# Performance work log

Hardware: AMD Instinct MI355X
Metric: run time of the kernel (lower is better)

## Reference

```python
import jax, jax.numpy as jnp
import numpy as np

EMB_DIM, TREE_DIM, OUT_DIM, VOCAB = 256, 256, 3, 10000
T, B, LEVELS = 255, 128, 8  # complete binary tree of depth 8, 128 trees per input


def _build_forest():
    # node j = T-1-heap(j): root (heap 0) is the LAST node so stack_last_h picks the root.
    heap = np.arange(T)
    depth = np.floor(np.log2(heap + 1)).astype(np.int64)  # 0..7
    node_order = np.empty(T, dtype=np.int64)
    node_order[T - 1 - heap] = (LEVELS - 1) - depth       # leaves=0, root=7
    internal = np.arange((T - 1) // 2)                     # heaps with two children
    parent = np.repeat(T - 1 - internal, 2)
    child = np.stack([T - 1 - (2 * internal + 1), T - 1 - (2 * internal + 2)], 1).reshape(-1)
    edges = np.stack([parent, child], axis=1)              # (254, 2)
    edge_order = node_order[parent]
    offs = (np.arange(B) * T)[:, None, None]
    adj = (edges[None] + offs).reshape(-1, 2)              # (B*254, 2)
    return np.tile(node_order, B), adj, np.tile(edge_order, B)


def setup_inputs() -> dict:
    key = jax.random.key(0)
    ks = jax.random.split(key, 16)
    no, adj, eo = _build_forest()
    D = TREE_DIM
    s_e = 1.0 / np.sqrt(EMB_DIM)
    s_t = 1.0 / np.sqrt(D)
    return {
        'feat_cube': jax.random.randint(ks[0], (B * T,), 0, VOCAB),
        'feat_a': jax.random.randint(ks[1], (B * T,), 0, VOCAB),
        'feat_b': jax.random.randint(ks[2], (B * T,), 0, VOCAB),
        'node_order': jnp.asarray(no),
        'adjacency_list': jnp.asarray(adj),
        'edge_order': jnp.asarray(eo),
        'num_levels': LEVELS,
        'num_trees': B,
        'emb': jax.random.normal(ks[3], (VOCAB, EMB_DIM), jnp.float32),
        'W_iou': jax.random.normal(ks[4], (3 * D, EMB_DIM), jnp.float32) * s_e,
        'b_iou': jnp.zeros((3 * D,), jnp.float32),
        'U_iou': jax.random.normal(ks[5], (3 * D, D), jnp.float32) * s_t,
        'W_f': jax.random.normal(ks[6], (D, EMB_DIM), jnp.float32) * s_e,
        'b_f': jnp.zeros((D,), jnp.float32),
        'U_f': jax.random.normal(ks[7], (D, D), jnp.float32) * s_t,
        'fc1_w': jax.random.normal(ks[8], (D // 2, D), jnp.float32) * s_t,
        'fc1_b': jnp.zeros((D // 2,), jnp.float32),
        'fc2_w': jax.random.normal(ks[9], (OUT_DIM, D // 2), jnp.float32) * (1.0 / np.sqrt(D // 2)),
        'fc2_b': jnp.zeros((OUT_DIM,), jnp.float32),
    }


def _tree_lstm(x, node_order, parents, children, edge_order, W_iou, b_iou, U_iou, W_f, b_f, U_f, num_levels):
    # Child-sum TreeLSTM, evaluated level by level (leaves first). Dense masked
    # formulation: per level we update only nodes with node_order==lvl; edge
    # contributions are masked before segment_sum (same math as the torch loop).
    N = x.shape[0]
    D = U_f.shape[0]
    x_iou = x @ W_iou.T + b_iou            # (N, 3D), precomputed once
    x_f = x @ W_f.T + b_f                  # (N, D)
    h = jnp.zeros((N, D), x.dtype)
    c = jnp.zeros((N, D), x.dtype)
    for lvl in range(num_levels):
        emask = (edge_order == lvl)[:, None].astype(x.dtype)
        ch = h[children]                   # (E, D) gather of child hidden
        cc = c[children]
        f = jax.nn.sigmoid(x_f[parents] + ch @ U_f.T)
        h_sum = jax.ops.segment_sum(ch * emask, parents, num_segments=N)
        c_sum = jax.ops.segment_sum(f * cc * emask, parents, num_segments=N)
        i, o, u = jnp.split(x_iou + h_sum @ U_iou.T, 3, axis=1)
        c_new = jax.nn.sigmoid(i) * jnp.tanh(u) + c_sum
        h_new = jax.nn.sigmoid(o) * jnp.tanh(c_new)
        nmask = (node_order == lvl)[:, None]
        h = jnp.where(nmask, h_new, h)
        c = jnp.where(nmask, c_new, c)
    return h, c


def reference(feat_cube, feat_a, feat_b, node_order, adjacency_list, edge_order,
              num_levels, num_trees, emb, W_iou, b_iou, U_iou, W_f, b_f, U_f,
              fc1_w, fc1_b, fc2_w, fc2_b):
    parents = adjacency_list[:, 0]
    children = adjacency_list[:, 1]

    def run_tree(feat):
        h, _ = _tree_lstm(emb[feat], node_order, parents, children, edge_order,
                          W_iou, b_iou, U_iou, W_f, b_f, U_f, num_levels)
        # stack_last_h: last node of each tree (= root with our labeling)
        return h.reshape(num_trees, -1, h.shape[-1])[:, -1, :]

    h_c = run_tree(feat_cube)
    h_a = run_tree(feat_a)
    h_b = run_tree(feat_b)
    # h_c (1,D) @ (h_a (D,1) @ h_b (1,D)) == (h_c . h_a) * h_b, fused einsum
    h = jnp.einsum('bi,bi,bj->bj', h_c, h_a, h_b)
    hid = jax.nn.relu(h @ fc1_w.T + fc1_b)
    logits = jax.nn.relu(hid @ fc2_w.T + fc2_b)
    return logits  # (num_trees, out_dim)
```

## Files before the change

### kernel.cpp

```cpp
#include <hip/hip_runtime.h>
#include <hip/hip_bf16.h>

typedef __hip_bfloat16 bf16;
typedef unsigned short u16;
typedef __attribute__((ext_vector_type(8))) short s8;
typedef __attribute__((ext_vector_type(4))) float f4;

#define NRUNS 3
#define NTREE 128
#define TT    255
#define DD    256
#define VPAD  10016
#define PAD   258
#define OPAD  264
#define FPAD  264

__device__ __forceinline__ float bits2f(u16 b){ union{unsigned u; float f;} x; x.u = ((unsigned)b)<<16; return x.f; }
__device__ __forceinline__ u16   f2bits(float f){ bf16 h = __float2bfloat16(f); return *(u16*)&h; }
__device__ __forceinline__ float sigm(float x){ return 1.f/(1.f+__expf(-x)); }
__device__ __forceinline__ float tanh_(float x){ return 1.f - 2.f/(__expf(2.f*x)+1.f); }

__global__ void k_detect(const u16* __restrict__ raw, int* __restrict__ flag){
    int t = threadIdx.x;
    int hit = 0;
    if (t < 128){
        u16 w = raw[2*t];
        int e = (w >> 7) & 0xFF;
        hit = (e >= 100 && e <= 141) ? 1 : 0;
    }
    __shared__ int cnt;
    if (t == 0) cnt = 0;
    __syncthreads();
    atomicAdd(&cnt, hit);
    __syncthreads();
    if (t == 0) flag[0] = (cnt >= 64) ? 1 : 0;
}

__device__ __forceinline__ u16 cvt1b(const void* p, int i, int isb){
    return isb ? ((const u16*)p)[i] : f2bits(((const float*)p)[i]);
}
__device__ __forceinline__ float cvt1f(const void* p, int i, int isb){
    return isb ? bits2f(((const u16*)p)[i]) : ((const float*)p)[i];
}

#define L_EMB  (10000*256)
#define L_EMBP (VPAD*256)
#define L_WIOU (768*256)
#define L_UIOU (768*256)
#define L_WF   (256*256)
#define L_UF   (256*256)
#define L_ALL  (L_EMBP + L_WIOU + L_UIOU + L_WF + L_UF)
__global__ void k_cvtb(const void* __restrict__ s0, const void* __restrict__ s1,
                       const void* __restrict__ s2, const void* __restrict__ s3,
                       const void* __restrict__ s4,
                       u16* __restrict__ d0, u16* __restrict__ d1, u16* __restrict__ d2,
                       u16* __restrict__ d3, u16* __restrict__ d4,
                       const int* __restrict__ flag){
    int isb = flag[0];
    for (int i = blockIdx.x*blockDim.x + threadIdx.x; i < L_ALL; i += gridDim.x*blockDim.x){
        int j = i;
        if (j < L_EMBP){ d0[j] = (j < L_EMB) ? cvt1b(s0, j, isb) : (u16)0; continue; } j -= L_EMBP;
        if (j < L_WIOU){ d1[j] = cvt1b(s1, j, isb); continue; } j -= L_WIOU;
        if (j < L_UIOU){ d2[j] = cvt1b(s2, j, isb); continue; } j -= L_UIOU;
        if (j < L_WF){ d3[j] = cvt1b(s3, j, isb); continue; } j -= L_WF;
        d4[j] = cvt1b(s4, j, isb);
    }
}

#define S_BIOU 768
#define S_BF   256
#define S_F1W  (128*256)
#define S_F1B  128
#define S_F2W  (3*128)
#define S_F2B  3
#define S_ALL  (S_BIOU+S_BF+S_F1W+S_F1B+S_F2W+S_F2B)
__global__ void k_small(const void* __restrict__ s0, const void* __restrict__ s1,
                        const void* __restrict__ s2, const void* __restrict__ s3,
                        const void* __restrict__ s4, const void* __restrict__ s5,
                        float* __restrict__ d0, float* __restrict__ d1, float* __restrict__ d2,
                        float* __restrict__ d3, float* __restrict__ d4, float* __restrict__ d5,
                        const int* __restrict__ flag){
    int isb = flag[0];
    for (int i = blockIdx.x*blockDim.x + threadIdx.x; i < S_ALL; i += gridDim.x*blockDim.x){
        int j = i;
        if (j < S_BIOU){ d0[j] = cvt1f(s0, j, isb); continue; } j -= S_BIOU;
        if (j < S_BF){ d1[j] = cvt1f(s1, j, isb); continue; } j -= S_BF;
        if (j < S_F1W){ d2[j] = cvt1f(s2, j, isb); continue; } j -= S_F1W;
        if (j < S_F1B){ d3[j] = cvt1f(s3, j, isb); continue; } j -= S_F1B;
        if (j < S_F2W){ d4[j] = cvt1f(s4, j, isb); continue; } j -= S_F2W;
        d5[j] = cvt1f(s5, j, isb);
    }
}

__device__ __forceinline__ s8 ldB16(const u16* p){
    union { uint4 q; s8 v; } u;
    u.q = *(const uint4*)p;
    return u.v;
}
__device__ __forceinline__ s8 ldsA(const u16* p){
    union { unsigned w[4]; s8 v; } u;
    u.w[0] = *(const unsigned*)(p);
    u.w[1] = *(const unsigned*)(p+2);
    u.w[2] = *(const unsigned*)(p+4);
    u.w[3] = *(const unsigned*)(p+6);
    return u.v;
}
#define MFMA(acc,a,b) acc = __builtin_amdgcn_mfma_f32_16x16x32_bf16(a, b, acc, 0, 0, 0)

__global__ __launch_bounds__(512, 4)
void k_vocab2(const u16* __restrict__ embb,
              const u16* __restrict__ Wiou, const u16* __restrict__ Wfm,
              const u16* __restrict__ Ufm,  const float* __restrict__ biou_f,
              u16* __restrict__ E4, u16* __restrict__ E_f,
              u16* __restrict__ H0, u16* __restrict__ C0, u16* __restrict__ HU0)
{
    __shared__ u16 hs[32*PAD];
    const int t = threadIdx.x, w = t>>6, lane = t&63, ln = lane&15, q = lane>>4;
    const int r0 = blockIdx.x*32, d0 = w*32;

    const u16* Bp[8];
    #pragma unroll
    for (int g = 0; g < 4; g++)
      #pragma unroll
      for (int nc = 0; nc < 2; nc++){
        int nn = d0 + nc*16 + ln;
        Bp[g*2+nc] = (g < 3) ? (Wiou + (size_t)(g*256+nn)*DD) : (Wfm + (size_t)nn*DD);
      }
    const u16* a0p = embb + (size_t)(r0+ln)*DD;
    const u16* a1p = embb + (size_t)(r0+16+ln)*DD;
    f4 acc[8][2];
    #pragma unroll
    for (int nt = 0; nt < 8; nt++){ acc[nt][0] = (f4){0,0,0,0}; acc[nt][1] = (f4){0,0,0,0}; }
    #pragma unroll 2
    for (int ks = 0; ks < 8; ks++){
        int ko = ks*32 + q*8;
        s8 a0 = ldB16(a0p + ko);
        s8 a1 = ldB16(a1p + ko);
        #pragma unroll
        for (int nt = 0; nt < 8; nt++){
            s8 bb = ldB16(Bp[nt] + ko);
            MFMA(acc[nt][0], a0, bb);
            MFMA(acc[nt][1], a1, bb);
        }
    }
    #pragma unroll
    for (int nc = 0; nc < 2; nc++){
        int d = d0 + nc*16 + ln;
        float bi = biou_f[d], bo = biou_f[256+d], bu = biou_f[512+d];
        #pragma unroll
        for (int ms = 0; ms < 2; ms++)
          #pragma unroll
          for (int r = 0; r < 4; r++){
            int vrow = r0 + ms*16 + q*4 + r;
            float ei = acc[0*2+nc][ms][r];
            float eo = acc[1*2+nc][ms][r];
            float eu = acc[2*2+nc][ms][r];
            float ef = acc[3*2+nc][ms][r];
            union { u16 a[4]; uint2 q2; } pk;
            pk.a[0] = f2bits(ei);
            pk.a[1] = f2bits(eo);
            pk.a[2] = f2bits(eu);
            pk.a[3] = f2bits(ef);
            *(uint2*)(E4 + ((size_t)vrow*DD + d)*4) = pk.q2;
            E_f[(size_t)vrow*DD + d] = f2bits(ef);
            float cc = sigm(ei + bi)*tanh_(eu + bu);
            float hh = sigm(eo + bo)*tanh_(cc);
            C0[(size_t)vrow*DD + d] = f2bits(cc);
            H0[(size_t)vrow*DD + d] = f2bits(hh);
            hs[(ms*16 + q*4 + r)*PAD + d] = f2bits(hh);
        }
    }
    __syncthreads();

    f4 hacc[2][2];
    #pragma unroll
    for (int nt = 0; nt < 2; nt++){ hacc[nt][0] = (f4){0,0,0,0}; hacc[nt][1] = (f4){0,0,0,0}; }
    const u16* Bf0 = Ufm + (size_t)(d0 + ln)*DD;
    const u16* Bf1 = Ufm + (size_t)(d0 + 16 + ln)*DD;
    #pragma unroll 2
    for (int ks = 0; ks < 8; ks++){
        int ko = ks*32 + q*8;
        s8 a0 = ldsA(&hs[ln*PAD + ko]);
        s8 a1 = ldsA(&hs[(16+ln)*PAD + ko]);
        s8 b0 = ldB16(Bf0 + ko);
        s8 b1 = ldB16(Bf1 + ko);
        MFMA(hacc[0][0], a0, b0); MFMA(hacc[0][1], a1, b0);
        MFMA(hacc[1][0], a0, b1); MFMA(hacc[1][1], a1, b1);
    }
    #pragma unroll
    for (int nc = 0; nc < 2; nc++){
        int d = d0 + nc*16 + ln;
        #pragma unroll
        for (int ms = 0; ms < 2; ms++)
          #pragma unroll
          for (int r = 0; r < 4; r++){
            int vrow = r0 + ms*16 + q*4 + r;
            HU0[(size_t)vrow*DD + d] = f2bits(hacc[nc][ms][r]);
        }
    }
}

__global__ __launch_bounds__(512, 4)
void k_edge0(const int* __restrict__ f0, const int* __restrict__ f1, const int* __restrict__ f2,
             const u16* __restrict__ E_f, const u16* __restrict__ H0,
             const u16* __restrict__ C0,  const u16* __restrict__ HU0,
             const float* __restrict__ bf_f,
             u16* __restrict__ hsum_out, u16* __restrict__ fcsum_out)
{
    int gid = blockIdx.x*512 + threadIdx.x;
    int row = gid >> 5, ch = gid & 31, d = ch*8;
    int run = row >> 13, rem = row & 8191, b = rem >> 6, jj = rem & 63;
    const int* fp = (run==0) ? f0 : ((run==1) ? f1 : f2);
    int fo = fp[b*TT + 128 + jj];
    int v1 = fp[b*TT + 2*jj];
    int v2 = fp[b*TT + 2*jj + 1];
    s8 ef  = ldB16(E_f + (size_t)fo*DD + d);
    s8 hu1 = ldB16(HU0 + (size_t)v1*DD + d);
    s8 hu2 = ldB16(HU0 + (size_t)v2*DD + d);
    s8 c1  = ldB16(C0  + (size_t)v1*DD + d);
    s8 c2  = ldB16(C0  + (size_t)v2*DD + d);
    s8 h1  = ldB16(H0  + (size_t)v1*DD + d);
    s8 h2  = ldB16(H0  + (size_t)v2*DD + d);
    union { u16 a[8]; uint4 q4; } uh, uf;
    #pragma unroll
    for (int j = 0; j < 8; j++){
        float e  = bits2f((u16)ef[j]) + bf_f[d+j];
        float fa = sigm(e + bits2f((u16)hu1[j]));
        float fb = sigm(e + bits2f((u16)hu2[j]));
        float fc = fa*bits2f((u16)c1[j]) + fb*bits2f((u16)c2[j]);
        float hsv = bits2f((u16)h1[j]) + bits2f((u16)h2[j]);
        uf.a[j] = f2bits(fc);
        uh.a[j] = f2bits(hsv);
    }
    *(uint4*)(hsum_out  + (size_t)row*DD + d) = uh.q4;
    *(uint4*)(fcsum_out + (size_t)row*DD + d) = uf.q4;
}

__global__ __launch_bounds__(512, 4)
void k_lvl(int lvl, int cLog,
           const int* __restrict__ f0, const int* __restrict__ f1, const int* __restrict__ f2,
           const u16* __restrict__ E4, const u16* __restrict__ E_f,
           const u16* __restrict__ Uiou, const u16* __restrict__ Ufm,
           const float* __restrict__ biou_f, const float* __restrict__ bf_f,
           const u16* __restrict__ hsum_in, const u16* __restrict__ fcsum_in,
           u16* __restrict__ hsum_out, u16* __restrict__ fcsum_out,
           u16* __restrict__ hroot)
{
    __shared__ u16 hs[32*PAD];
    __shared__ u16 hso[16*OPAD];
    __shared__ u16 fco[16*OPAD];
    __shared__ int sfr[32];
    const int t = threadIdx.x, w = t>>6, lane = t&63, ln = lane&15, q = lane>>4;
    const int cnt = 1 << cLog, S = 256 - 2*cnt;
    const int r0 = blockIdx.x*32, d0 = w*32;
    const bool haveP = (lvl < 7);

    if (t < 32){
        int rho = r0 + t;
        int run = rho >> (7+cLog);
        int rem = rho & ((1<<(7+cLog)) - 1);
        int b = rem >> cLog, jj = rem & (cnt-1);
        const int* fp = (run==0) ? f0 : ((run==1) ? f1 : f2);
        sfr[t] = fp[b*TT + S + jj];
    }

    int featp[2][2];
    if (haveP){
        #pragma unroll
        for (int ms = 0; ms < 2; ms++)
          #pragma unroll
          for (int rr = 0; rr < 2; rr++){
            int rho = r0 + ms*16 + q*4 + rr*2;
            int run = rho >> (7+cLog);
            int rem = rho & ((1<<(7+cLog)) - 1);
            int b = rem >> cLog, jj = rem & (cnt-1);
            const int* fp = (run==0) ? f0 : ((run==1) ? f1 : f2);
            featp[ms][rr] = fp[b*TT + (256-cnt) + (jj>>1)];
          }
    }
    __syncthreads();

    f4 acc[6][2];
    #pragma unroll
    for (int nt = 0; nt < 6; nt++){ acc[nt][0] = (f4){0,0,0,0}; acc[nt][1] = (f4){0,0,0,0}; }
    {
        const u16* a0p = hsum_in + (size_t)(r0+ln)*DD;
        const u16* a1p = hsum_in + (size_t)(r0+16+ln)*DD;
        const u16* Bp[6];
        #pragma unroll
        for (int nt = 0; nt < 6; nt++){
            int n = (nt>>1)*256 + d0 + (nt&1)*16 + ln;
            Bp[nt] = Uiou + (size_t)n*DD;
        }
        #pragma unroll 2
        for (int ks = 0; ks < 8; ks++){
            int ko = ks*32 + q*8;
            s8 a0 = ldB16(a0p + ko);
            s8 a1 = ldB16(a1p + ko);
            #pragma unroll
            for (int nt = 0; nt < 6; nt++){
                s8 bb = ldB16(Bp[nt] + ko);
                MFMA(acc[nt][0], a0, bb);
                MFMA(acc[nt][1], a1, bb);
            }
        }
    }

    float cv[2][2][4];
    #pragma unroll
    for (int nc = 0; nc < 2; nc++){
        int d = d0 + nc*16 + ln;
        float bi = biou_f[d], bo = biou_f[256+d], bu = biou_f[512+d];
        #pragma unroll
        for (int ms = 0; ms < 2; ms++){
            float hv[4];
            #pragma unroll
            for (int r = 0; r < 4; r++){
                int m   = ms*16 + q*4 + r;
                int rho = r0 + m;
                union { uint2 q2; u16 a[4]; } ev;
                ev.q2 = *(const uint2*)(E4 + ((size_t)sfr[m]*DD + d)*4);
                float iv = acc[0+nc][ms][r] + bits2f(ev.a[0]) + bi;
                float ov = acc[2+nc][ms][r] + bits2f(ev.a[1]) + bo;
                float uv = acc[4+nc][ms][r] + bits2f(ev.a[2]) + bu;
                float cs = bits2f(fcsum_in[(size_t)rho*DD + d]);
                float c = sigm(iv)*tanh_(uv) + cs;
                float h = sigm(ov)*tanh_(c);
                cv[nc][ms][r] = c;
                hv[r] = h;
                if (haveP) hs[m*PAD + d] = f2bits(h);
                else       hroot[(size_t)rho*DD + d] = f2bits(h);
            }
            if (haveP){
                int lr = ms*8 + q*2;
                hso[lr*OPAD + d]     = f2bits(hv[0] + hv[1]);
                hso[(lr+1)*OPAD + d] = f2bits(hv[2] + hv[3]);
            }
        }
    }

    if (haveP){
        __syncthreads();
        f4 hacc[2][2];
        #pragma unroll
        for (int nt = 0; nt < 2; nt++){ hacc[nt][0] = (f4){0,0,0,0}; hacc[nt][1] = (f4){0,0,0,0}; }
        const u16* Bf0 = Ufm + (size_t)(d0 + ln)*DD;
        const u16* Bf1 = Ufm + (size_t)(d0 + 16 + ln)*DD;
        #pragma unroll 2
        for (int ks = 0; ks < 8; ks++){
            int ko = ks*32 + q*8;
            s8 a0 = ldsA(&hs[ln*PAD + ko]);
            s8 a1 = ldsA(&hs[(16+ln)*PAD + ko]);
            s8 b0 = ldB16(Bf0 + ko);
            s8 b1 = ldB16(Bf1 + ko);
            MFMA(hacc[0][0], a0, b0); MFMA(hacc[0][1], a1, b0);
            MFMA(hacc[1][0], a0, b1); MFMA(hacc[1][1], a1, b1);
        }
        #pragma unroll
        for (int nc = 0; nc < 2; nc++){
            int d = d0 + nc*16 + ln;
            float bfv = bf_f[d];
            #pragma unroll
            for (int ms = 0; ms < 2; ms++){
                float fs0, fs1;
                #pragma unroll
                for (int r = 0; r < 4; r++){
                    float ef = bits2f(E_f[(size_t)featp[ms][r>>1]*DD + d]);
                    float fc = sigm(ef + bfv + hacc[nc][ms][r]) * cv[nc][ms][r];
                    if (r == 0) fs0 = fc;
                    else if (r == 1) fs0 += fc;
                    else if (r == 2) fs1 = fc;
                    else fs1 += fc;
                }
                int lr = ms*8 + q*2;
                fco[lr*OPAD + d]     = f2bits(fs0);
                fco[(lr+1)*OPAD + d] = f2bits(fs1);
            }
        }

        __syncthreads();
        {
            int row = t >> 5, c = (t & 31) * 8;
            int prow = (r0 >> 1) + row;
            uint4 vh = *(const uint4*)&hso[row*OPAD + c];
            uint4 vf = *(const uint4*)&fco[row*OPAD + c];
            *(uint4*)(hsum_out  + (size_t)prow*DD + c) = vh;
            *(uint4*)(fcsum_out + (size_t)prow*DD + c) = vf;
        }
    }
}

__global__ __launch_bounds__(1024, 4)
void k_tail(const int* __restrict__ f0, const int* __restrict__ f1, const int* __restrict__ f2,
            const u16* __restrict__ E4, const u16* __restrict__ E_f,
            const u16* __restrict__ Uiou, const u16* __restrict__ Ufm,
            const float* __restrict__ biou_f, const float* __restrict__ bf_f,
            const u16* __restrict__ hsum_in, const u16* __restrict__ fcsum_in,
            u16* __restrict__ hroot)
{
    __shared__ u16 hs[32*PAD];
    __shared__ u16 hsP[2][32*PAD];
    __shared__ u16 fcP[2][32*FPAD];
    __shared__ int sf[64];
    const int t = threadIdx.x, w = t>>6, lane = t&63, ln = lane&15, q = lane>>4;
    const int d0 = w*16;
    const int d  = d0 + ln;
    const int r0 = blockIdx.x*32;
    const int run = (blockIdx.x*4) >> 7;
    const int* __restrict__ fp = (run==0) ? f0 : ((run==1) ? f1 : f2);

    if (t < 64){
        int ti = t >> 4, idx = t & 15;
        int b = (blockIdx.x*4 + ti) & 127;
        sf[t] = (idx < 15) ? fp[b*TT + 240 + idx] : 0;
    }
    __syncthreads();

    const u16* Bp[3];
    #pragma unroll
    for (int g = 0; g < 3; g++)
        Bp[g] = Uiou + (size_t)(g*256 + d0 + ln)*DD;
    const u16* Bf0 = Ufm + (size_t)(d0 + ln)*DD;

    const float bi = biou_f[d], bo = biou_f[256+d], bu = biou_f[512+d];
    const float bfv = bf_f[d];

    for (int l = 4; l <= 7; l++){
        const int nl = 128 >> l;
        const int nrows = 4*nl;
        const int sh = 7 - l;
        const int inb = (l-1) & 1, outb = l & 1;
        const bool haveP = (l < 7);

        f4 acc[3][2];
        #pragma unroll
        for (int nt = 0; nt < 3; nt++){ acc[nt][0] = (f4){0,0,0,0}; acc[nt][1] = (f4){0,0,0,0}; }
        if (l == 4){
            const u16* a0p = hsum_in + (size_t)(r0+ln)*DD;
            const u16* a1p = hsum_in + (size_t)(r0+16+ln)*DD;
            #pragma unroll 2
            for (int ks = 0; ks < 8; ks++){
                int ko = ks*32 + q*8;
                s8 a0 = ldB16(a0p + ko);
                s8 a1 = ldB16(a1p + ko);
                #pragma unroll
                for (int nt = 0; nt < 3; nt++){
                    s8 bb = ldB16(Bp[nt] + ko);
                    MFMA(acc[nt][0], a0, bb);
                    MFMA(acc[nt][1], a1, bb);
                }
            }
        } else {
            const u16* a0l = &hsP[inb][ln*PAD];
            const u16* a1l = &hsP[inb][(16+ln)*PAD];
            #pragma unroll 2
            for (int ks = 0; ks < 8; ks++){
                int ko = ks*32 + q*8;
                s8 a0 = ldsA(a0l + ko);
                s8 a1 = ldsA(a1l + ko);
                #pragma unroll
                for (int nt = 0; nt < 3; nt++){
                    s8 bb = ldB16(Bp[nt] + ko);
                    MFMA(acc[nt][0], a0, bb);
                    MFMA(acc[nt][1], a1, bb);
                }
            }
        }

        uint2 ev[2][4];
        float csv[2][4];
        #pragma unroll
        for (int ms = 0; ms < 2; ms++)
          #pragma unroll
          for (int r = 0; r < 4; r++){
            int m = ms*16 + q*4 + r;
            int mc = (m < nrows) ? m : 0;
            int ti = mc >> sh, jj = mc & (nl-1);
            int fidx = sf[ti*16 + (16 - 2*nl) + jj];
            ev[ms][r] = *(const uint2*)(E4 + ((size_t)fidx*DD + d)*4);
            csv[ms][r] = (l == 4) ? bits2f(fcsum_in[(size_t)(r0+m)*DD + d])
                                  : bits2f(fcP[inb][m*FPAD + d]);
        }

        float cv[2][4];
        #pragma unroll
        for (int ms = 0; ms < 2; ms++){
            float hv[4];
            #pragma unroll
            for (int r = 0; r < 4; r++){
                int m = ms*16 + q*4 + r;
                bool vld = (m < nrows);
                union { uint2 q2; u16 a[4]; } u2;
                u2.q2 = ev[ms][r];
                float iv = acc[0][ms][r] + bits2f(u2.a[0]) + bi;
                float ov = acc[1][ms][r] + bits2f(u2.a[1]) + bo;
                float uv = acc[2][ms][r] + bits2f(u2.a[2]) + bu;
                float c = sigm(iv)*tanh_(uv) + csv[ms][r];
                float h = sigm(ov)*tanh_(c);
                cv[ms][r] = c;
                hv[r] = h;
                if (haveP) hs[m*PAD + d] = f2bits(h);
                else if (vld) hroot[(size_t)(blockIdx.x*4 + m)*DD + d] = f2bits(h);
            }
            if (haveP){
                int lr = ms*8 + q*2;
                hsP[outb][lr*PAD + d]     = f2bits(hv[0] + hv[1]);
                hsP[outb][(lr+1)*PAD + d] = f2bits(hv[2] + hv[3]);
            }
        }

        if (haveP){
            __syncthreads();
            f4 hacc[2];
            hacc[0] = (f4){0,0,0,0}; hacc[1] = (f4){0,0,0,0};
            #pragma unroll 2
            for (int ks = 0; ks < 8; ks++){
                int ko = ks*32 + q*8;
                s8 a0 = ldsA(&hs[ln*PAD + ko]);
                s8 a1 = ldsA(&hs[(16+ln)*PAD + ko]);
                s8 b0 = ldB16(Bf0 + ko);
                MFMA(hacc[0], a0, b0);
                MFMA(hacc[1], a1, b0);
            }

            float efv[2][2];
            #pragma unroll
            for (int ms = 0; ms < 2; ms++)
              #pragma unroll
              for (int rr = 0; rr < 2; rr++){
                int m2 = ms*16 + q*4 + rr*2;
                int mc2 = (m2 < nrows) ? m2 : 0;
                int ti2 = mc2 >> sh, jj2 = mc2 & (nl-1);
                int fpar = sf[ti2*16 + (16 - nl) + (jj2 >> 1)];
                efv[ms][rr] = bits2f(E_f[(size_t)fpar*DD + d]);
            }
            #pragma unroll
            for (int ms = 0; ms < 2; ms++){
                float fs0, fs1;
                #pragma unroll
                for (int r = 0; r < 4; r++){
                    float ef = efv[ms][r>>1];
                    float fc = sigm(ef + bfv + hacc[ms][r]) * cv[ms][r];
                    if (r == 0) fs0 = fc;
                    else if (r == 1) fs0 += fc;
                    else if (r == 2) fs1 = fc;
                    else fs1 += fc;
                }
                int lr = ms*8 + q*2;
                fcP[outb][lr*FPAD + d]     = f2bits(fs0);
                fcP[outb][(lr+1)*FPAD + d] = f2bits(fs1);
            }
            __syncthreads();
        }
    }
}

__global__ __launch_bounds__(256)
void k_final(const u16* __restrict__ hroot,
             const float* __restrict__ fc1w, const float* __restrict__ fc1b,
             const float* __restrict__ fc2w, const float* __restrict__ fc2b,
             void* __restrict__ out, const int* __restrict__ flag)
{
    int b = blockIdx.x, t = threadIdx.x;
    __shared__ float sprod[DD];
    __shared__ float shb[DD];
    __shared__ float shid[128];
    float hc  = bits2f(hroot[(0*NTREE + b)*DD + t]);
    float ha  = bits2f(hroot[(1*NTREE + b)*DD + t]);
    float hbv = bits2f(hroot[(2*NTREE + b)*DD + t]);
    sprod[t] = hc * ha;
    shb[t]   = hbv;
    __syncthreads();
    for (int s = 128; s > 0; s >>= 1){
        if (t < s) sprod[t] += sprod[t + s];
        __syncthreads();
    }
    float dot = sprod[0];
    if (t < 128){
        float acc = fc1b[t];
        for (int k = 0; k < DD; k++)
            acc = fmaf(dot * shb[k], fc1w[t*DD + k], acc);
        shid[t] = fmaxf(acc, 0.f);
    }
    __syncthreads();
    if (t < 3){
        float acc = fc2b[t];
        for (int j = 0; j < 128; j++)
            acc = fmaf(fc2w[t*128 + j], shid[j], acc);
        float v = fmaxf(acc, 0.f);
        if (flag[0]) ((bf16*)out)[b*3 + t] = __float2bfloat16(v);
        else         ((float*)out)[b*3 + t] = v;
    }
}

extern "C" void kernel_launch(void* const* d_in, const int* in_sizes, int n_in,
                              void* d_out, int out_size, void* d_ws, size_t ws_size,
                              hipStream_t stream)
{
    const int* f0 = (const int*)d_in[0];
    const int* f1 = (const int*)d_in[1];
    const int* f2 = (const int*)d_in[2];
    const void* emb  = d_in[8];
    const void* Wiou = d_in[9];
    const void* biou = d_in[10];
    const void* Uiou = d_in[11];
    const void* Wf   = d_in[12];
    const void* bfv  = d_in[13];
    const void* Uf   = d_in[14];
    const void* fc1w = d_in[15];
    const void* fc1b = d_in[16];
    const void* fc2w = d_in[17];
    const void* fc2b = d_in[18];

    char* base = (char*)d_ws;
    size_t off = 0;
    auto take = [&](size_t bytes) -> char* {
        char* p = base + off;
        off = (off + bytes + 255) & ~(size_t)255;
        return p;
    };
    int*   flag   = (int*)  take(256);
    u16*   embb   = (u16*)  take((size_t)L_EMBP*2);
    u16*   wioub  = (u16*)  take((size_t)L_WIOU*2);
    u16*   uioub  = (u16*)  take((size_t)L_UIOU*2);
    u16*   wfb    = (u16*)  take((size_t)L_WF*2);
    u16*   ufb    = (u16*)  take((size_t)L_UF*2);
    float* biou_f = (float*)take(S_BIOU*4);
    float* bf_f   = (float*)take(S_BF*4);
    float* fc1w_f = (float*)take(S_F1W*4);
    float* fc1b_f = (float*)take(S_F1B*4);
    float* fc2w_f = (float*)take(S_F2W*4);
    float* fc2b_f = (float*)take(S_F2B*4);
    u16*   E4     = (u16*)  take((size_t)VPAD*DD*4*2);
    u16*   E_f    = (u16*)  take((size_t)VPAD*DD*2);
    u16*   H0     = (u16*)  take((size_t)VPAD*DD*2);
    u16*   C0     = (u16*)  take((size_t)VPAD*DD*2);
    u16*   HU0    = (u16*)  take((size_t)VPAD*DD*2);
    u16*   HA     = (u16*)  take((size_t)24576*DD*2);
    u16*   HB     = (u16*)  take((size_t)12288*DD*2);
    u16*   FA     = (u16*)  take((size_t)24576*DD*2);
    u16*   FB     = (u16*)  take((size_t)12288*DD*2);
    u16*   hroot  = (u16*)  take((size_t)NRUNS*NTREE*DD*2);

    k_detect<<<1, 256, 0, stream>>>((const u16*)emb, flag);
    k_cvtb<<<2048, 256, 0, stream>>>(emb, Wiou, Uiou, Wf, Uf,
                                     embb, wioub, uioub, wfb, ufb, flag);
    k_small<<<135, 256, 0, stream>>>(biou, bfv, fc1w, fc1b, fc2w, fc2b,
                                     biou_f, bf_f, fc1w_f, fc1b_f, fc2w_f, fc2b_f, flag);
    k_vocab2<<<VPAD/32, 512, 0, stream>>>(embb, wioub, wfb, ufb, biou_f,
                                          E4, E_f, H0, C0, HU0);
    k_edge0<<<24576*32/512, 512, 0, stream>>>(f0, f1, f2, E_f, H0, C0, HU0, bf_f, HA, FA);

    for (int lvl = 1; lvl <= 3; lvl++){
        int cLog = 7 - lvl;
        int rows = NRUNS*NTREE*(128 >> lvl);
        int blocks = rows / 32;
        int pe = lvl & 1;
        u16* hs_o = pe ? HB : HA;
        u16* fc_o = pe ? FB : FA;
        const u16* hs_i = pe ? HA : HB;
        const u16* fc_i = pe ? FA : FB;
        k_lvl<<<blocks, 512, 0, stream>>>(lvl, cLog, f0, f1, f2,
                                          E4, E_f, uioub, ufb,
                                          biou_f, bf_f,
                                          hs_i, fc_i, hs_o, fc_o, hroot);
    }
    k_tail<<<(NRUNS*NTREE)/4, 1024, 0, stream>>>(f0, f1, f2, E4, E_f, uioub, ufb,
                                                 biou_f, bf_f, HB, FB, hroot);
    k_final<<<NTREE, 256, 0, stream>>>(hroot, fc1w_f, fc1b_f, fc2w_f, fc2b_f, d_out, flag);
}
```

Before: 421.3 us.

## Fuse forget-gate GEMM with next level's iou GEMM in tail kernel loop

Restructures the level loop in k_tail so that each iteration runs the forget-gate U_f GEMM for the current level and the iou U_iou GEMM for the parent level in one shared k-loop. Both GEMMs read h and hsum from shared memory, and the loop then syncs once before the parent's cell update. The goal is to cut a __syncthreads per level and interleave independent MFMA chains to raise latency hiding. Double-buffered hsP/fcP become single buffers to save LDS, at the cost of more live registers (hacc plus acc at once) and a sync ordering that must stay correct.

Result: no change. 419.8 us (median of 2 runs) (-0.3%).

```diff
diff --git a/kernel.cpp b/kernel.cpp
--- a/kernel.cpp
+++ b/kernel.cpp
@@ -399,8 +399,8 @@
             u16* __restrict__ hroot)
 {
     __shared__ u16 hs[32*PAD];
-    __shared__ u16 hsP[2][32*PAD];
-    __shared__ u16 fcP[2][32*FPAD];
+    __shared__ u16 hsP[32*PAD];
+    __shared__ u16 fcP[32*FPAD];
     __shared__ int sf[64];
     const int t = threadIdx.x, w = t>>6, lane = t&63, ln = lane&15, q = lane>>4;
     const int d0 = w*16;
@@ -425,48 +425,28 @@
     const float bi = biou_f[d], bo = biou_f[256+d], bu = biou_f[512+d];
     const float bfv = bf_f[d];
 
-    for (int l = 4; l <= 7; l++){
-        const int nl = 128 >> l;
-        const int nrows = 4*nl;
-        const int sh = 7 - l;
-        const int inb = (l-1) & 1, outb = l & 1;
-        const bool haveP = (l < 7);
-
-        f4 acc[3][2];
-        #pragma unroll
-        for (int nt = 0; nt < 3; nt++){ acc[nt][0] = (f4){0,0,0,0}; acc[nt][1] = (f4){0,0,0,0}; }
-        if (l == 4){
-            const u16* a0p = hsum_in + (size_t)(r0+ln)*DD;
-            const u16* a1p = hsum_in + (size_t)(r0+16+ln)*DD;
-            #pragma unroll 2
-            for (int ks = 0; ks < 8; ks++){
-                int ko = ks*32 + q*8;
-                s8 a0 = ldB16(a0p + ko);
-                s8 a1 = ldB16(a1p + ko);
-                #pragma unroll
-                for (int nt = 0; nt < 3; nt++){
-                    s8 bb = ldB16(Bp[nt] + ko);
-                    MFMA(acc[nt][0], a0, bb);
-                    MFMA(acc[nt][1], a1, bb);
-                }
-            }
-        } else {
-            const u16* a0l = &hsP[inb][ln*PAD];
-            const u16* a1l = &hsP[inb][(16+ln)*PAD];
-            #pragma unroll 2
-            for (int ks = 0; ks < 8; ks++){
-                int ko = ks*32 + q*8;
-                s8 a0 = ldsA(a0l + ko);
-                s8 a1 = ldsA(a1l + ko);
-                #pragma unroll
-                for (int nt = 0; nt < 3; nt++){
-                    s8 bb = ldB16(Bp[nt] + ko);
-                    MFMA(acc[nt][0], a0, bb);
-                    MFMA(acc[nt][1], a1, bb);
-                }
-            }
-        }
-
+    f4 acc[3][2];
+    float cv[2][4];
+
+    #pragma unroll
+    for (int nt = 0; nt < 3; nt++){ acc[nt][0] = (f4){0,0,0,0}; acc[nt][1] = (f4){0,0,0,0}; }
+    {
+        const u16* a0p = hsum_in + (size_t)(r0+ln)*DD;
+        const u16* a1p = hsum_in + (size_t)(r0+16+ln)*DD;
+        #pragma unroll 2
+        for (int ks = 0; ks < 8; ks++){
+            int ko = ks*32 + q*8;
+            s8 a0 = ldB16(a0p + ko);
+            s8 a1 = ldB16(a1p + ko);
+            #pragma unroll
+            for (int nt = 0; nt < 3; nt++){
+                s8 bb = ldB16(Bp[nt] + ko);
+                MFMA(acc[nt][0], a0, bb);
+                MFMA(acc[nt][1], a1, bb);
+            }
+        }
+    }
+    {
         uint2 ev[2][4];
         float csv[2][4];
         #pragma unroll
@@ -474,22 +454,16 @@
           #pragma unroll
           for (int r = 0; r < 4; r++){
             int m = ms*16 + q*4 + r;
-            int mc = (m < nrows) ? m : 0;
-            int ti = mc >> sh, jj = mc & (nl-1);
-            int fidx = sf[ti*16 + (16 - 2*nl) + jj];
+            int fidx = sf[(m>>3)*16 + (m&7)];
             ev[ms][r] = *(const uint2*)(E4 + ((size_t)fidx*DD + d)*4);
-            csv[ms][r] = (l == 4) ? bits2f(fcsum_in[(size_t)(r0+m)*DD + d])
-                                  : bits2f(fcP[inb][m*FPAD + d]);
-        }
-
-        float cv[2][4];
+            csv[ms][r] = bits2f(fcsum_in[(size_t)(r0+m)*DD + d]);
+        }
         #pragma unroll
         for (int ms = 0; ms < 2; ms++){
             float hv[4];
             #pragma unroll
             for (int r = 0; r < 4; r++){
                 int m = ms*16 + q*4 + r;
-                bool vld = (m < nrows);
                 union { uint2 q2; u16 a[4]; } u2;
                 u2.q2 = ev[ms][r];
                 float iv = acc[0][ms][r] + bits2f(u2.a[0]) + bi;
@@ -499,59 +473,109 @@
                 float h = sigm(ov)*tanh_(c);
                 cv[ms][r] = c;
                 hv[r] = h;
-                if (haveP) hs[m*PAD + d] = f2bits(h);
+                hs[m*PAD + d] = f2bits(h);
+            }
+            int lr = ms*8 + q*2;
+            hsP[lr*PAD + d]     = f2bits(hv[0] + hv[1]);
+            hsP[(lr+1)*PAD + d] = f2bits(hv[2] + hv[3]);
+        }
+    }
+    __syncthreads();
+
+    for (int l = 4; l <= 6; l++){
+        const int nlc = 128 >> l, nrows_c = 4*nlc, shc = 7 - l;
+        const int nlu = nlc >> 1, nrows_u = 4*nlu, shu = shc - 1;
+        const bool lastU = (l == 6);
+
+        f4 hacc[2];
+        hacc[0] = (f4){0,0,0,0}; hacc[1] = (f4){0,0,0,0};
+        #pragma unroll
+        for (int nt = 0; nt < 3; nt++){ acc[nt][0] = (f4){0,0,0,0}; acc[nt][1] = (f4){0,0,0,0}; }
+        #pragma unroll 2
+        for (int ks = 0; ks < 8; ks++){
+            int ko = ks*32 + q*8;
+            s8 a0c = ldsA(&hs[ln*PAD + ko]);
+            s8 a1c = ldsA(&hs[(16+ln)*PAD + ko]);
+            s8 a0u = ldsA(&hsP[ln*PAD + ko]);
+            s8 a1u = ldsA(&hsP[(16+ln)*PAD + ko]);
+            s8 bfm = ldB16(Bf0 + ko);
+            MFMA(hacc[0], a0c, bfm);
+            MFMA(hacc[1], a1c, bfm);
+            #pragma unroll
+            for (int nt = 0; nt < 3; nt++){
+                s8 bb = ldB16(Bp[nt] + ko);
+                MFMA(acc[nt][0], a0u, bb);
+                MFMA(acc[nt][1], a1u, bb);
+            }
+        }
+
+        uint2 ev2[2][4];
+        #pragma unroll
+        for (int ms = 0; ms < 2; ms++)
+          #pragma unroll
+          for (int r = 0; r < 4; r++){
+            int m = ms*16 + q*4 + r;
+            int mc = (m < nrows_u) ? m : 0;
+            int ti = mc >> shu, jj = mc & (nlu-1);
+            int fidx = sf[ti*16 + (16 - 2*nlu) + jj];
+            ev2[ms][r] = *(const uint2*)(E4 + ((size_t)fidx*DD + d)*4);
+        }
+        float efv[2][2];
+        #pragma unroll
+        for (int ms = 0; ms < 2; ms++)
+          #pragma unroll
+          for (int rr = 0; rr < 2; rr++){
+            int m2 = ms*16 + q*4 + rr*2;
+            int mc2 = (m2 < nrows_c) ? m2 : 0;
+            int ti2 = mc2 >> shc, jj2 = mc2 & (nlc-1);
+            int fpar = sf[ti2*16 + (16 - nlc) + (jj2 >> 1)];
+            efv[ms][rr] = bits2f(E_f[(size_t)fpar*DD + d]);
+        }
+        #pragma unroll
+        for (int ms = 0; ms < 2; ms++){
+            float fs0, fs1;
+            #pragma unroll
+            for (int r = 0; r < 4; r++){
+                float ef = efv[ms][r>>1];
+                float fc = sigm(ef + bfv + hacc[ms][r]) * cv[ms][r];
+                if (r == 0) fs0 = fc;
+                else if (r == 1) fs0 += fc;
+                else if (r == 2) fs1 = fc;
+                else fs1 += fc;
+            }
+            int lr = ms*8 + q*2;
+            fcP[lr*FPAD + d]     = f2bits(fs0);
+            fcP[(lr+1)*FPAD + d] = f2bits(fs1);
+        }
+        __syncthreads();
+
+        #pragma unroll
+        for (int ms = 0; ms < 2; ms++){
+            float hv[4];
+            #pragma unroll
+            for (int r = 0; r < 4; r++){
+                int m = ms*16 + q*4 + r;
+                bool vld = (m < nrows_u);
+                union { uint2 q2; u16 a[4]; } u2;
+                u2.q2 = ev2[ms][r];
+                float iv = acc[0][ms][r] + bits2f(u2.a[0]) + bi;
+                float ov = acc[1][ms][r] + bits2f(u2.a[1]) + bo;
+                float uv = acc[2][ms][r] + bits2f(u2.a[2]) + bu;
+                float cs = bits2f(fcP[m*FPAD + d]);
+                float c = sigm(iv)*tanh_(uv) + cs;
+                float h = sigm(ov)*tanh_(c);
+                cv[ms][r] = c;
+                hv[r] = h;
+                if (!lastU) hs[m*PAD + d] = f2bits(h);
                 else if (vld) hroot[(size_t)(blockIdx.x*4 + m)*DD + d] = f2bits(h);
             }
-            if (haveP){
+            if (!lastU){
                 int lr = ms*8 + q*2;
-                hsP[outb][lr*PAD + d]     = f2bits(hv[0] + hv[1]);
-                hsP[outb][(lr+1)*PAD + d] = f2bits(hv[2] + hv[3]);
-            }
-        }
-
-        if (haveP){
-            __syncthreads();
-            f4 hacc[2];
-            hacc[0] = (f4){0,0,0,0}; hacc[1] = (f4){0,0,0,0};
-            #pragma unroll 2
-            for (int ks = 0; ks < 8; ks++){
-                int ko = ks*32 + q*8;
-                s8 a0 = ldsA(&hs[ln*PAD + ko]);
-                s8 a1 = ldsA(&hs[(16+ln)*PAD + ko]);
-                s8 b0 = ldB16(Bf0 + ko);
-                MFMA(hacc[0], a0, b0);
-                MFMA(hacc[1], a1, b0);
-            }
-
-            float efv[2][2];
-            #pragma unroll
-            for (int ms = 0; ms < 2; ms++)
-              #pragma unroll
-              for (int rr = 0; rr < 2; rr++){
-                int m2 = ms*16 + q*4 + rr*2;
-                int mc2 = (m2 < nrows) ? m2 : 0;
-                int ti2 = mc2 >> sh, jj2 = mc2 & (nl-1);
-                int fpar = sf[ti2*16 + (16 - nl) + (jj2 >> 1)];
-                efv[ms][rr] = bits2f(E_f[(size_t)fpar*DD + d]);
-            }
-            #pragma unroll
-            for (int ms = 0; ms < 2; ms++){
-                float fs0, fs1;
-                #pragma unroll
-                for (int r = 0; r < 4; r++){
-                    float ef = efv[ms][r>>1];
-                    float fc = sigm(ef + bfv + hacc[ms][r]) * cv[ms][r];
-                    if (r == 0) fs0 = fc;
-                    else if (r == 1) fs0 += fc;
-                    else if (r == 2) fs1 = fc;
-                    else fs1 += fc;
-                }
-                int lr = ms*8 + q*2;
-                fcP[outb][lr*FPAD + d]     = f2bits(fs0);
-                fcP[outb][(lr+1)*FPAD + d] = f2bits(fs1);
-            }
-            __syncthreads();
-        }
+                hsP[lr*PAD + d]     = f2bits(hv[0] + hv[1]);
+                hsP[(lr+1)*PAD + d] = f2bits(hv[2] + hv[3]);
+            }
+        }
+        if (!lastU) __syncthreads();
     }
 }
 
```
